# Kernel tuning notes

Measured on AMD Instinct MI355X. Metric: run time of the kernel, lower is better.

## Reference

```python
import jax, jax.numpy as jnp
import numpy as np

PS = 8  # window_size
LOCAL = 16  # split channels

def conv1x1(x, w, b):
    return jnp.einsum('oi,bihw->bohw', w, x) + b[None, :, None, None]

def dynamic_local(x, w1, b1, w2, b2, k):
    # x: (B, C, H, W); dynamic per-(batch,channel) depthwise conv with generated kernels
    B, C, H, W = x.shape
    pooled = x.mean((2, 3))                      # (B, C) adaptive avg pool to 1x1
    h = jax.nn.relu(pooled @ w1.T + b1)
    kern = (h @ w2.T + b2).reshape(B, C, k, k)   # per-sample depthwise kernels
    def per_batch(xb, kb):
        return jax.lax.conv_general_dilated(
            xb[None], kb[:, None], (1, 1), 'SAME',
            feature_group_count=C,
            dimension_numbers=('NCHW', 'OIHW', 'NCHW'))[0]
    return jax.vmap(per_batch)(x, kern)

def channel_layernorm(x, w, b, eps=1e-6):
    # LayerNorm over channel dim (torch module's non-channels_last path)
    u = x.mean(1, keepdims=True)
    s = ((x - u) ** 2).mean(1, keepdims=True)
    xn = (x - u) / jnp.sqrt(s + eps)
    return w[None, :, None, None] * xn + b[None, :, None, None]

def fsas(x, hid_w, hid_b, dw_w, dw_b, ln_w, ln_b, out_w, out_b):
    hidden = conv1x1(x, hid_w, hid_b)
    mid = hidden.shape[1]
    dw = jax.lax.conv_general_dilated(
        hidden, dw_w[:, None], (1, 1), 'SAME',
        feature_group_count=mid,
        dimension_numbers=('NCHW', 'OIHW', 'NCHW')) + dw_b[None, :, None, None]
    q, k, v = jnp.split(dw, 3, axis=1)
    B, C, H, W = q.shape
    def patch(t):
        # (B,C,H,W) -> (B,C,H/ps,W/ps,ps,ps)
        return t.reshape(B, C, H // PS, PS, W // PS, PS).transpose(0, 1, 2, 4, 3, 5)
    qf = jnp.fft.rfft2(patch(q))
    kf = jnp.fft.rfft2(patch(k))
    out = jnp.fft.irfft2(qf * kf, s=(PS, PS))
    out = out.transpose(0, 1, 2, 4, 3, 5).reshape(B, C, H, W)
    out = channel_layernorm(out, ln_w, ln_b)
    return conv1x1(v * out, out_w, out_b)


def setup_inputs() -> dict:
    key = jax.random.key(0)
    ks = jax.random.split(key, 12)
    s = 0.02
    return {
        'x': jax.random.normal(ks[0], (4, 64, 256, 256), jnp.float32),
        'dl1_w1': jax.random.normal(ks[1], (16, 16), jnp.float32) * s,
        'dl1_b1': jnp.zeros((16,), jnp.float32),
        'dl1_w2': jax.random.normal(ks[2], (144, 16), jnp.float32) * s,
        'dl1_b2': jnp.zeros((144,), jnp.float32),
        'dl2_w1': jax.random.normal(ks[3], (16, 16), jnp.float32) * s,
        'dl2_b1': jnp.zeros((16,), jnp.float32),
        'dl2_w2': jax.random.normal(ks[4], (400, 16), jnp.float32) * s,
        'dl2_b2': jnp.zeros((400,), jnp.float32),
        'fs_hid_w': jax.random.normal(ks[5], (144, 48), jnp.float32) * s,
        'fs_hid_b': jnp.zeros((144,), jnp.float32),
        'fs_dw_w': jax.random.normal(ks[6], (144, 3, 3), jnp.float32) * s,
        'fs_dw_b': jnp.zeros((144,), jnp.float32),
        'fs_ln_w': jnp.ones((48,), jnp.float32),
        'fs_ln_b': jnp.zeros((48,), jnp.float32),
        'fs_out_w': jax.random.normal(ks[7], (48, 48), jnp.float32) * s,
        'fs_out_b': jnp.zeros((48,), jnp.float32),
        'last_w': jax.random.normal(ks[8], (64, 64), jnp.float32) * s,
        'last_b': jnp.zeros((64,), jnp.float32),
    }


def reference(x, dl1_w1, dl1_b1, dl1_w2, dl1_b2, dl2_w1, dl2_b1, dl2_w2, dl2_b2,
              fs_hid_w, fs_hid_b, fs_dw_w, fs_dw_b, fs_ln_w, fs_ln_b,
              fs_out_w, fs_out_b, last_w, last_b):
    x1, x2 = x[:, :LOCAL], x[:, LOCAL:]
    x1 = dynamic_local(x1, dl1_w1, dl1_b1, dl1_w2, dl1_b2, 3)
    x1 = dynamic_local(x1, dl2_w1, dl2_b1, dl2_w2, dl2_b2, 5)
    x2 = fsas(x2, fs_hid_w, fs_hid_b, fs_dw_w, fs_dw_b, fs_ln_w, fs_ln_b, fs_out_w, fs_out_b)
    return conv1x1(jnp.concatenate([x1, x2], axis=1), last_w, last_b)
```

## Files before the change

### kernel.cpp

```cpp
#include <hip/hip_runtime.h>

typedef _Float16 h2 __attribute__((ext_vector_type(2)));
typedef _Float16 h4 __attribute__((ext_vector_type(4)));
typedef _Float16 h8 __attribute__((ext_vector_type(8)));
typedef float f4 __attribute__((ext_vector_type(4)));
typedef unsigned int u32;
typedef u32 u32x2 __attribute__((ext_vector_type(2)));
typedef u32 u32x4 __attribute__((ext_vector_type(4)));

__device__ __forceinline__ h2 bch2(u32 v) { return __builtin_bit_cast(h2, v); }

__device__ __forceinline__ float warpsum(float v) {
    for (int off = 32; off > 0; off >>= 1) v += __shfl_down(v, off);
    return v;
}

__device__ __forceinline__ int sswz(int p, int k) {
    return p * 64 + ((((k >> 3) ^ (p >> 3)) & 7) << 3) + (k & 7);
}

__global__ __launch_bounds__(256) void k_prep(const float* __restrict__ hid_w,
                                              const float* __restrict__ out_w,
                                              const float* __restrict__ last_w,
                                              _Float16* __restrict__ hwH,
                                              _Float16* __restrict__ owlwH) {
    int t = blockIdx.x * 256 + threadIdx.x;
    int stride = gridDim.x * 256;
    for (int i = t; i < 10368; i += stride) {
        int n = i / 72, k = i - n * 72;
        hwH[i] = (k < 48) ? (_Float16)hid_w[n * 48 + k] : (_Float16)0.f;
    }
    for (int i = t; i < 3456; i += stride) {
        int n = i / 72, k = i - n * 72;
        owlwH[i] = (k < 48) ? (_Float16)out_w[n * 48 + k] : (_Float16)0.f;
    }
    for (int i = t; i < 4608; i += stride) {
        int n = i / 72, k = i - n * 72;
        owlwH[3456 + i] = (k < 64) ? (_Float16)last_w[n * 64 + k] : (_Float16)0.f;
    }
}

__global__ __launch_bounds__(256) void k_pool(const float* __restrict__ x, float* __restrict__ pooled1) {
    int bid = blockIdx.x;
    int b = bid >> 4, c = bid & 15;
    const float* base = x + (size_t)(b * 64 + c) * 65536;
    float s = 0.f;
    for (int i = threadIdx.x; i < 16384; i += 256) {
        float4 v = ((const float4*)base)[i];
        s += v.x + v.y + v.z + v.w;
    }
    __shared__ float red[4];
    s = warpsum(s);
    if ((threadIdx.x & 63) == 0) red[threadIdx.x >> 6] = s;
    __syncthreads();
    if (threadIdx.x == 0) pooled1[bid] = (red[0] + red[1] + red[2] + red[3]) * (1.f / 65536.f);
}

__global__ __launch_bounds__(256) void k_kern1(const float* __restrict__ pooled1,
                                               const float* __restrict__ w1, const float* __restrict__ b1,
                                               const float* __restrict__ w2, const float* __restrict__ b2,
                                               float* __restrict__ kern1) {
    __shared__ float h[64];
    int t = threadIdx.x;
    if (t < 64) {
        int b = t >> 4, j = t & 15;
        float a = b1[j];
        for (int i = 0; i < 16; ++i) a += pooled1[b * 16 + i] * w1[j * 16 + i];
        h[t] = fmaxf(a, 0.f);
    }
    __syncthreads();
    for (int i = t; i < 576; i += 256) {
        int b = i / 144, o = i - b * 144;
        float a = b2[o];
        for (int j = 0; j < 16; ++j) a += h[b * 16 + j] * w2[o * 16 + j];
        kern1[i] = a;
    }
}

__global__ __launch_bounds__(256) void k_dw3(const float* __restrict__ x,
                                             const float* __restrict__ kern1,
                                             float* __restrict__ y1, float* __restrict__ rowsum) {
    __shared__ float tile[10][258];
    __shared__ float red[8][4];
    int bid = blockIdx.x;
    int rb = bid & 31, bc = bid >> 5;
    int b = bc >> 4, c = bc & 15;
    int row0 = rb << 3;
    int col = threadIdx.x;
    const float* xc = x + ((size_t)(b * 64 + c) << 16);
#pragma unroll
    for (int j = 0; j < 10; ++j) {
        int r = row0 - 1 + j;
        tile[j][col + 1] = ((unsigned)r < 256u) ? xc[(r << 8) + col] : 0.f;
    }
    if (col < 10) { tile[col][0] = 0.f; tile[col][257] = 0.f; }
    const float* k9 = kern1 + b * 144 + c * 9;
    float kk[9];
#pragma unroll
    for (int i = 0; i < 9; ++i) kk[i] = k9[i];
    __syncthreads();
#pragma unroll
    for (int j = 0; j < 8; ++j) {
        float acc = 0.f;
#pragma unroll
        for (int dy = 0; dy < 3; ++dy)
#pragma unroll
            for (int dx = 0; dx < 3; ++dx)
                acc += kk[dy * 3 + dx] * tile[j + dy][col + dx];
        y1[((size_t)bc << 16) + ((row0 + j) << 8) + col] = acc;
        float s = warpsum(acc);
        if ((col & 63) == 0) red[j][col >> 6] = s;
    }
    __syncthreads();
    if (col < 8) rowsum[bc * 256 + row0 + col] = red[col][0] + red[col][1] + red[col][2] + red[col][3];
}

__global__ __launch_bounds__(256) void k_kern2(const float* __restrict__ rowsum,
                                               const float* __restrict__ w1, const float* __restrict__ b1,
                                               const float* __restrict__ w2, const float* __restrict__ b2,
                                               float* __restrict__ kern2) {
    __shared__ float ps[256];
    __shared__ float p2[64];
    __shared__ float h[64];
    int t = threadIdx.x;
    {
        int pair = t >> 2, seg = t & 3;
        const float* rs = rowsum + pair * 256 + seg * 64;
        float s = 0.f;
        for (int j = 0; j < 64; ++j) s += rs[j];
        ps[t] = s;
    }
    __syncthreads();
    if (t < 64) p2[t] = (ps[t * 4] + ps[t * 4 + 1] + ps[t * 4 + 2] + ps[t * 4 + 3]) * (1.f / 65536.f);
    __syncthreads();
    if (t < 64) {
        int b = t >> 4, j = t & 15;
        float a = b1[j];
        for (int i = 0; i < 16; ++i) a += p2[b * 16 + i] * w1[j * 16 + i];
        h[t] = fmaxf(a, 0.f);
    }
    __syncthreads();
    for (int i = t; i < 1600; i += 256) {
        int b = i / 400, o = i - b * 400;
        float a = b2[o];
        for (int j = 0; j < 16; ++j) a += h[b * 16 + j] * w2[o * 16 + j];
        kern2[i] = a;
    }
}

__global__ __launch_bounds__(256) void k_dw5(const float* __restrict__ y1,
                                             const float* __restrict__ kern2,
                                             float* __restrict__ x1o) {
    __shared__ float tile[12][260];
    int bid = blockIdx.x;
    int rb = bid & 31, bc = bid >> 5;
    int b = bc >> 4, c = bc & 15;
    int row0 = rb << 3;
    int col = threadIdx.x;
    const float* yc = y1 + ((size_t)bc << 16);
#pragma unroll
    for (int j = 0; j < 12; ++j) {
        int r = row0 - 2 + j;
        tile[j][col + 2] = ((unsigned)r < 256u) ? yc[(r << 8) + col] : 0.f;
    }
    if (col < 12) { tile[col][0] = 0.f; tile[col][1] = 0.f; tile[col][258] = 0.f; tile[col][259] = 0.f; }
    const float* k25 = kern2 + b * 400 + c * 25;
    float kk[25];
#pragma unroll
    for (int i = 0; i < 25; ++i) kk[i] = k25[i];
    __syncthreads();
#pragma unroll
    for (int j = 0; j < 8; ++j) {
        float acc = 0.f;
#pragma unroll
        for (int dy = 0; dy < 5; ++dy)
#pragma unroll
            for (int dx = 0; dx < 5; ++dx)
                acc += kk[dy * 5 + dx] * tile[j + dy][col + dx];
        x1o[((size_t)bc << 16) + ((row0 + j) << 8) + col] = acc;
    }
}

__global__ __launch_bounds__(512, 6) void k_fsas(const float* __restrict__ x,
                                                 const _Float16* __restrict__ hwH, const float* __restrict__ hid_b,
                                                 const float* __restrict__ dw_w, const float* __restrict__ dw_b,
                                                 const float* __restrict__ ln_w, const float* __restrict__ ln_b,
                                                 const _Float16* __restrict__ owlwH, const float* __restrict__ out_b,
                                                 const float* __restrict__ last_b,
                                                 const float* __restrict__ x1o, float* __restrict__ out) {
    __shared__ __align__(16) _Float16 Sbig[17856];
    __shared__ __align__(16) _Float16 qk[6144];
    __shared__ __align__(16) float pstat[128];

    _Float16* Abuf  = Sbig;
    _Float16* hbuf  = Sbig;
    _Float16* fbuf  = Sbig;
    float*    lnp   = (float*)(Sbig + 4608);
    _Float16* outb  = Sbig + 6656;
    _Float16* qbuf  = qk;
    _Float16* kbuf  = qk + 3072;
    _Float16* sbufA = qk;

    int tid = threadIdx.x;
    int lane = tid & 63;
    int wave = __builtin_amdgcn_readfirstlane(tid >> 6);
    int bid = blockIdx.x;
    int swz = ((bid & 7) << 9) | (bid >> 3);
    int b = swz >> 10;
    int rem = swz & 1023;
    int row0 = (rem >> 5) << 3, col0 = (rem & 31) << 3;

    int l16 = lane & 15, lhi = lane >> 4;
    int mb = wave * 16 + (lhi << 2);
    bool vok[4];
#pragma unroll
    for (int r = 0; r < 4; ++r) {
        int m = mb + r;
        int yv = m / 12, xv = m - yv * 12;
        vok[r] = (m < 120) && (xv < 10) &&
                 ((unsigned)(row0 - 1 + yv) < 256u) && ((unsigned)(col0 - 1 + xv) < 256u);
    }

    if (tid < 480) {
        int k2 = tid / 20, r20 = tid - (tid / 20) * 20;
        int y = r20 >> 1, xh = r20 & 1;
        int gy = row0 - 1 + y;
        bool rowok = (unsigned)gy < 256u;
        const float* xa = x + ((size_t)(b * 64 + 16 + 2 * k2) << 16) + ((size_t)(gy & 255) << 8);
        const float* xb = xa + 65536;
#pragma unroll
        for (int xx = 0; xx < 6; ++xx) {
            int xv = xh * 6 + xx;
            int gx = col0 - 1 + xv;
            bool ok = rowok && (xv < 10) && ((unsigned)gx < 256u);
            float va = ok ? xa[gx] : 0.f;
            float vb = ok ? xb[gx] : 0.f;
            *(h2*)(Abuf + (y * 12 + xv) * 72 + 2 * k2) = (h2){(_Float16)va, (_Float16)vb};
        }
    }
    if (tid < 240) {
        int p = tid >> 1, kb = 48 + ((tid & 1) << 3);
        *(h8*)(Abuf + p * 72 + kb) = (h8)(_Float16)0.f;
    }
    __syncthreads();

    int arow = wave * 16 + l16;
    h8 a0 = *(const h8*)(Abuf + arow * 72 + (lhi << 3));
    h8 a1 = *(const h8*)(Abuf + arow * 72 + 32 + (lhi << 3));
    __syncthreads();

    float xr[8];
    int fpx = lane, fgrp = wave - 6;
    if (wave >= 6) {
        size_t gp = ((size_t)(row0 + (fpx >> 3)) << 8) + col0 + (fpx & 7);
#pragma unroll
        for (int j = 0; j < 8; ++j)
            xr[j] = x1o[((size_t)(b * 16 + fgrp * 8 + j) << 16) + gp];
    }

#pragma unroll
    for (int nt = 0; nt < 9; ++nt) {
        const _Float16* wr = hwH + (nt * 16 + l16) * 72 + (lhi << 3);
        h8 b0 = *(const h8*)(wr);
        h8 b1 = *(const h8*)(wr + 32);
        float bias = hid_b[nt * 16 + l16];
        f4 acc = {bias, bias, bias, bias};
        acc = __builtin_amdgcn_mfma_f32_16x16x32_f16(a0, b0, acc, 0, 0, 0);
        acc = __builtin_amdgcn_mfma_f32_16x16x32_f16(a1, b1, acc, 0, 0, 0);
        int n_l = nt * 16 + l16;
        if (mb < 120) {
            h2 p0 = {vok[0] ? (_Float16)acc[0] : (_Float16)0.f, vok[1] ? (_Float16)acc[1] : (_Float16)0.f};
            h2 p1 = {vok[2] ? (_Float16)acc[2] : (_Float16)0.f, vok[3] ? (_Float16)acc[3] : (_Float16)0.f};
            *(h2*)(hbuf + n_l * 124 + mb) = p0;
            *(h2*)(hbuf + n_l * 124 + mb + 2) = p1;
        }
    }
    __syncthreads();

    int dch = tid >> 3, drow = tid & 7;
    h8 vreg;
    auto dw_row = [&](int ch, int row, float o[8]) {
        const float* dwp = dw_w + ch * 9;
        float bias = dw_b[ch];
#pragma unroll
        for (int xx = 0; xx < 8; ++xx) o[xx] = bias;
        const _Float16* hb = hbuf + ch * 124 + row * 12;
#pragma unroll
        for (int dy = 0; dy < 3; ++dy) {
            u32x2 A2 = *(const u32x2*)(hb + dy * 12);
            u32x2 B2 = *(const u32x2*)(hb + dy * 12 + 4);
            u32 r89 = *(const u32*)(hb + dy * 12 + 8);
            u32 r01 = A2.x, r23 = A2.y, r45 = B2.x, r67 = B2.y;
            u32 s12 = __builtin_amdgcn_alignbit(r23, r01, 16);
            u32 s34 = __builtin_amdgcn_alignbit(r45, r23, 16);
            u32 s56 = __builtin_amdgcn_alignbit(r67, r45, 16);
            u32 s78 = __builtin_amdgcn_alignbit(r89, r67, 16);
            _Float16 w0 = (_Float16)dwp[dy * 3], w1 = (_Float16)dwp[dy * 3 + 1], w2 = (_Float16)dwp[dy * 3 + 2];
            h2 w01 = {w0, w1};
            h2 w2lo = {w2, (_Float16)0.f};
            h2 w2hi = {(_Float16)0.f, w2};
            o[0] = __builtin_amdgcn_fdot2(w01, bch2(r01), o[0], false);
            o[0] = __builtin_amdgcn_fdot2(w2lo, bch2(r23), o[0], false);
            o[1] = __builtin_amdgcn_fdot2(w01, bch2(s12), o[1], false);
            o[1] = __builtin_amdgcn_fdot2(w2lo, bch2(s34), o[1], false);
            o[2] = __builtin_amdgcn_fdot2(w01, bch2(r23), o[2], false);
            o[2] = __builtin_amdgcn_fdot2(w2lo, bch2(r45), o[2], false);
            o[3] = __builtin_amdgcn_fdot2(w01, bch2(s34), o[3], false);
            o[3] = __builtin_amdgcn_fdot2(w2lo, bch2(s56), o[3], false);
            o[4] = __builtin_amdgcn_fdot2(w01, bch2(r45), o[4], false);
            o[4] = __builtin_amdgcn_fdot2(w2lo, bch2(r67), o[4], false);
            o[5] = __builtin_amdgcn_fdot2(w01, bch2(s56), o[5], false);
            o[5] = __builtin_amdgcn_fdot2(w2lo, bch2(s78), o[5], false);
            o[6] = __builtin_amdgcn_fdot2(w01, bch2(r67), o[6], false);
            o[6] = __builtin_amdgcn_fdot2(w2lo, bch2(r89), o[6], false);
            o[7] = __builtin_amdgcn_fdot2(w01, bch2(s78), o[7], false);
            o[7] = __builtin_amdgcn_fdot2(w2hi, bch2(r89), o[7], false);
        }
    };
    if (tid < 384) {
        float oq[8];
        dw_row(dch, drow, oq);
        h8 qv;
#pragma unroll
        for (int xx = 0; xx < 8; ++xx) qv[xx] = (_Float16)oq[xx];
        *(h8*)(qbuf + dch * 64 + drow * 8) = qv;
        float ov[8];
        dw_row(96 + dch, drow, ov);
#pragma unroll
        for (int xx = 0; xx < 8; ++xx) vreg[xx] = (_Float16)ov[xx];
    } else {
        int j0 = (tid - 384) * 3;
#pragma unroll
        for (int i = 0; i < 3; ++i) {
            int j = j0 + i;
            int kc = j >> 3, kr = j & 7;
            float ok8[8];
            dw_row(48 + kc, kr, ok8);
            h8 krv;
#pragma unroll
            for (int t2 = 0; t2 < 8; ++t2) krv[t2] = (_Float16)ok8[(8 - t2) & 7];
            *(h8*)(kbuf + kc * 64 + kr * 8) = krv;
        }
    }
    __syncthreads();

    float co[8];
    if (tid < 384) {
        int ch = dch, m = drow;
#pragma unroll
        for (int n = 0; n < 8; ++n) co[n] = 0.f;
#pragma unroll
        for (int i8 = 0; i8 < 8; ++i8) {
            int r = (m - i8) & 7;
            u32x4 qv = *(const u32x4*)(qbuf + ch * 64 + i8 * 8);
            u32x4 ev = *(const u32x4*)(kbuf + ch * 64 + r * 8);
            h2 qp[4] = {bch2(qv.x), bch2(qv.y), bch2(qv.z), bch2(qv.w)};
            h2 ep[4] = {bch2(ev.x), bch2(ev.y), bch2(ev.z), bch2(ev.w)};
            h2 op[4] = {bch2(__builtin_amdgcn_alignbit(ev.x, ev.w, 16)),
                        bch2(__builtin_amdgcn_alignbit(ev.y, ev.x, 16)),
                        bch2(__builtin_amdgcn_alignbit(ev.z, ev.y, 16)),
                        bch2(__builtin_amdgcn_alignbit(ev.w, ev.z, 16))};
#pragma unroll
            for (int u = 0; u < 4; ++u)
#pragma unroll
                for (int a = 0; a < 4; ++a) {
                    co[2 * u]     = __builtin_amdgcn_fdot2(qp[a], ep[(a - u) & 3], co[2 * u], false);
                    co[2 * u + 1] = __builtin_amdgcn_fdot2(qp[a], op[(a - u) & 3], co[2 * u + 1], false);
                }
        }
#pragma unroll
        for (int v = 0; v < 4; ++v)
            *(h2*)(outb + dch * 66 + drow * 8 + 2 * v) = (h2){(_Float16)co[2 * v], (_Float16)co[2 * v + 1]};
    } else {
        h8 fv;
#pragma unroll
        for (int j = 0; j < 8; ++j) fv[j] = (_Float16)xr[j];
        *(h8*)(fbuf + fpx * 72 + fgrp * 8) = fv;
    }
    __syncthreads();

    {
        int px = tid & 63, g = tid >> 6;
        float s = 0.f, ss = 0.f;
#pragma unroll
        for (int cc = 0; cc < 6; ++cc) {
            float v = (float)outb[(g * 6 + cc) * 66 + px];
            s += v; ss += v * v;
        }
        lnp[g * 64 + px] = s;
        lnp[512 + g * 64 + px] = ss;
    }
    __syncthreads();
    if (tid < 64) {
        float s = 0.f, ss = 0.f;
#pragma unroll
        for (int g = 0; g < 8; ++g) { s += lnp[g * 64 + tid]; ss += lnp[512 + g * 64 + tid]; }
        float mu = s * (1.f / 48.f);
        float var = ss * (1.f / 48.f) - mu * mu;
        pstat[tid * 2] = mu;
        pstat[tid * 2 + 1] = rsqrtf(var + 1e-6f);
    }
    __syncthreads();

    if (tid < 384) {
        float lw = ln_w[dch], lb = ln_b[dch];
        const float* ps = pstat + drow * 16;
#pragma unroll
        for (int n = 0; n < 8; ++n) {
            float mu = ps[2 * n], inv = ps[2 * n + 1];
            float lnv = lw * ((co[n] - mu) * inv) + lb;
            sbufA[sswz(drow * 8 + n, dch)] = (_Float16)((float)vreg[n] * lnv);
        }
    }
    *(h2*)(sbufA + sswz(lane, 48 + (wave << 1))) = (h2){(_Float16)0.f, (_Float16)0.f};
    __syncthreads();

    for (int t = wave; t < 12; t += 8) {
        int mt = t / 3, nt = t - mt * 3;
        int row5 = mt * 16 + l16;
        h8 c0 = *(const h8*)(sbufA + sswz(row5, lhi << 3));
        h8 c1 = *(const h8*)(sbufA + sswz(row5, 32 + (lhi << 3)));
        h8 d0 = *(const h8*)(owlwH + nt * 1152 + l16 * 72 + (lhi << 3));
        h8 d1 = *(const h8*)(owlwH + nt * 1152 + l16 * 72 + 32 + (lhi << 3));
        float bias = out_b[nt * 16 + l16];
        f4 acc = {bias, bias, bias, bias};
        acc = __builtin_amdgcn_mfma_f32_16x16x32_f16(c0, d0, acc, 0, 0, 0);
        acc = __builtin_amdgcn_mfma_f32_16x16x32_f16(c1, d1, acc, 0, 0, 0);
        int n5 = nt * 16 + l16;
        int pb = mt * 16 + (lhi << 2);
#pragma unroll
        for (int r = 0; r < 4; ++r)
            fbuf[(pb + r) * 72 + 16 + n5] = (_Float16)acc[r];
    }
    __syncthreads();

    for (int t = wave; t < 16; t += 8) {
        int mt = t >> 2, nt = t & 3;
        int row6 = mt * 16 + l16;
        h8 c0 = *(const h8*)(fbuf + row6 * 72 + (lhi << 3));
        h8 c1 = *(const h8*)(fbuf + row6 * 72 + 32 + (lhi << 3));
        h8 d0 = *(const h8*)(owlwH + 3456 + nt * 1152 + l16 * 72 + (lhi << 3));
        h8 d1 = *(const h8*)(owlwH + 3456 + nt * 1152 + l16 * 72 + 32 + (lhi << 3));
        float bias = last_b[nt * 16 + l16];
        f4 acc = {bias, bias, bias, bias};
        acc = __builtin_amdgcn_mfma_f32_16x16x32_f16(c0, d0, acc, 0, 0, 0);
        acc = __builtin_amdgcn_mfma_f32_16x16x32_f16(c1, d1, acc, 0, 0, 0);
        int ch = nt * 16 + l16;
        int px0 = mt * 16 + (lhi << 2);
        float4 val = {acc[0], acc[1], acc[2], acc[3]};
        *(float4*)(out + ((size_t)(b * 64 + ch) << 16) + ((size_t)(row0 + (px0 >> 3)) << 8) + col0 + (px0 & 7)) = val;
    }
}

extern "C" void kernel_launch(void* const* d_in, const int* in_sizes, int n_in,
                              void* d_out, int out_size, void* d_ws, size_t ws_size,
                              hipStream_t stream) {
    const float* x      = (const float*)d_in[0];
    const float* dl1_w1 = (const float*)d_in[1];
    const float* dl1_b1 = (const float*)d_in[2];
    const float* dl1_w2 = (const float*)d_in[3];
    const float* dl1_b2 = (const float*)d_in[4];
    const float* dl2_w1 = (const float*)d_in[5];
    const float* dl2_b1 = (const float*)d_in[6];
    const float* dl2_w2 = (const float*)d_in[7];
    const float* dl2_b2 = (const float*)d_in[8];
    const float* hid_w  = (const float*)d_in[9];
    const float* hid_b  = (const float*)d_in[10];
    const float* dw_w   = (const float*)d_in[11];
    const float* dw_b   = (const float*)d_in[12];
    const float* ln_w   = (const float*)d_in[13];
    const float* ln_b   = (const float*)d_in[14];
    const float* out_w  = (const float*)d_in[15];
    const float* out_b  = (const float*)d_in[16];
    const float* last_w = (const float*)d_in[17];
    const float* last_b = (const float*)d_in[18];
    float* out = (float*)d_out;

    float* ws      = (float*)d_ws;
    float* pooled1 = ws;
    float* kern1   = ws + 64;
    float* rowsum  = ws + 1024;
    float* kern2   = ws + 17408;
    _Float16* hwH   = (_Float16*)(ws + 19008);
    _Float16* owlwH = (_Float16*)(ws + 24192);
    float* y1      = ws + 32768;
    float* x1o     = ws + 32768 + 4194304;

    k_prep <<<8,    256, 0, stream>>>(hid_w, out_w, last_w, hwH, owlwH);
    k_pool <<<64,   256, 0, stream>>>(x, pooled1);
    k_kern1<<<1,    256, 0, stream>>>(pooled1, dl1_w1, dl1_b1, dl1_w2, dl1_b2, kern1);
    k_dw3  <<<2048, 256, 0, stream>>>(x, kern1, y1, rowsum);
    k_kern2<<<1,    256, 0, stream>>>(rowsum, dl2_w1, dl2_b1, dl2_w2, dl2_b2, kern2);
    k_dw5  <<<2048, 256, 0, stream>>>(y1, kern2, x1o);
    k_fsas <<<4096, 512, 0, stream>>>(x, hwH, hid_b, dw_w, dw_b, ln_w, ln_b,
                                      owlwH, out_b, last_b, x1o, out);
}
```

Measured before the change: 167.2 us.

## Fold fsas output projection into final 1x1 conv and compute layernorm stats via shuffles

Precomputes last_w[:,16:] @ out_w and a combined bias in the prep kernel, which removes the separate out-projection MFMA stage and one barrier from the fused kernel. Per-pixel layernorm sums are now reduced with wave-level xor shuffles inside the circular-convolution waves rather than through a staging buffer, two LDS passes and extra syncs. The folded weights are rounded to fp16 after the product, so numerics shift slightly, and the shuffle reduction adds register pressure in the convolution waves.

```diff
diff --git a/kernel.cpp b/kernel.cpp
--- a/kernel.cpp
+++ b/kernel.cpp
@@ -22,21 +22,31 @@
 __global__ __launch_bounds__(256) void k_prep(const float* __restrict__ hid_w,
                                               const float* __restrict__ out_w,
                                               const float* __restrict__ last_w,
+                                              const float* __restrict__ out_b,
+                                              const float* __restrict__ last_b,
                                               _Float16* __restrict__ hwH,
-                                              _Float16* __restrict__ owlwH) {
+                                              _Float16* __restrict__ lwC,
+                                              float* __restrict__ bias_comb) {
     int t = blockIdx.x * 256 + threadIdx.x;
     int stride = gridDim.x * 256;
     for (int i = t; i < 10368; i += stride) {
         int n = i / 72, k = i - n * 72;
         hwH[i] = (k < 48) ? (_Float16)hid_w[n * 48 + k] : (_Float16)0.f;
     }
-    for (int i = t; i < 3456; i += stride) {
-        int n = i / 72, k = i - n * 72;
-        owlwH[i] = (k < 48) ? (_Float16)out_w[n * 48 + k] : (_Float16)0.f;
-    }
-    for (int i = t; i < 4608; i += stride) {
-        int n = i / 72, k = i - n * 72;
-        owlwH[3456 + i] = (k < 64) ? (_Float16)last_w[n * 64 + k] : (_Float16)0.f;
+    for (int i = t; i < 4096; i += stride) {
+        int n = i >> 6, k = i & 63;
+        float v;
+        if (k < 16) v = last_w[n * 64 + k];
+        else {
+            v = 0.f;
+            for (int o = 0; o < 48; ++o) v += last_w[n * 64 + 16 + o] * out_w[o * 48 + (k - 16)];
+        }
+        lwC[i] = (_Float16)v;
+    }
+    for (int n = t; n < 64; n += stride) {
+        float v = last_b[n];
+        for (int o = 0; o < 48; ++o) v += last_w[n * 64 + 16 + o] * out_b[o];
+        bias_comb[n] = v;
     }
 }
 
@@ -185,21 +195,17 @@
                                                  const _Float16* __restrict__ hwH, const float* __restrict__ hid_b,
                                                  const float* __restrict__ dw_w, const float* __restrict__ dw_b,
                                                  const float* __restrict__ ln_w, const float* __restrict__ ln_b,
-                                                 const _Float16* __restrict__ owlwH, const float* __restrict__ out_b,
-                                                 const float* __restrict__ last_b,
+                                                 const _Float16* __restrict__ lwC, const float* __restrict__ bias_comb,
                                                  const float* __restrict__ x1o, float* __restrict__ out) {
     __shared__ __align__(16) _Float16 Sbig[17856];
     __shared__ __align__(16) _Float16 qk[6144];
-    __shared__ __align__(16) float pstat[128];
-
-    _Float16* Abuf  = Sbig;
-    _Float16* hbuf  = Sbig;
-    _Float16* fbuf  = Sbig;
-    float*    lnp   = (float*)(Sbig + 4608);
-    _Float16* outb  = Sbig + 6656;
-    _Float16* qbuf  = qk;
-    _Float16* kbuf  = qk + 3072;
-    _Float16* sbufA = qk;
+
+    _Float16* Abuf = Sbig;
+    _Float16* hbuf = Sbig;
+    _Float16* fbuf = Sbig;
+    float*    lnp2 = (float*)(Sbig + 4608);
+    _Float16* qbuf = qk;
+    _Float16* kbuf = qk + 3072;
 
     int tid = threadIdx.x;
     int lane = tid & 63;
@@ -250,9 +256,9 @@
     __syncthreads();
 
     float xr[8];
-    int fpx = lane, fgrp = wave - 6;
+    int fgrp = wave - 6;
     if (wave >= 6) {
-        size_t gp = ((size_t)(row0 + (fpx >> 3)) << 8) + col0 + (fpx & 7);
+        size_t gp = ((size_t)(row0 + (lane >> 3)) << 8) + col0 + (lane & 7);
 #pragma unroll
         for (int j = 0; j < 8; ++j)
             xr[j] = x1o[((size_t)(b * 16 + fgrp * 8 + j) << 16) + gp];
@@ -368,80 +374,66 @@
                     co[2 * u + 1] = __builtin_amdgcn_fdot2(qp[a], op[(a - u) & 3], co[2 * u + 1], false);
                 }
         }
-#pragma unroll
-        for (int v = 0; v < 4; ++v)
-            *(h2*)(outb + dch * 66 + drow * 8 + 2 * v) = (h2){(_Float16)co[2 * v], (_Float16)co[2 * v + 1]};
+        float s[8], ss[8];
+#pragma unroll
+        for (int n = 0; n < 8; ++n) { s[n] = co[n]; ss[n] = co[n] * co[n]; }
+#pragma unroll
+        for (int off = 8; off < 64; off <<= 1) {
+#pragma unroll
+            for (int n = 0; n < 8; ++n) {
+                s[n] += __shfl_xor(s[n], off);
+                ss[n] += __shfl_xor(ss[n], off);
+            }
+        }
+        int c8 = lane >> 3, mm = lane & 7;
+        int p = mm * 8 + c8;
+        float2 pv = {0.f, 0.f};
+#pragma unroll
+        for (int n = 0; n < 8; ++n) if (n == c8) { pv.x = s[n]; pv.y = ss[n]; }
+        *(float2*)(lnp2 + wave * 128 + p * 2) = pv;
     } else {
         h8 fv;
 #pragma unroll
         for (int j = 0; j < 8; ++j) fv[j] = (_Float16)xr[j];
-        *(h8*)(fbuf + fpx * 72 + fgrp * 8) = fv;
-    }
-    __syncthreads();
-
-    {
-        int px = tid & 63, g = tid >> 6;
-        float s = 0.f, ss = 0.f;
-#pragma unroll
-        for (int cc = 0; cc < 6; ++cc) {
-            float v = (float)outb[(g * 6 + cc) * 66 + px];
-            s += v; ss += v * v;
-        }
-        lnp[g * 64 + px] = s;
-        lnp[512 + g * 64 + px] = ss;
-    }
-    __syncthreads();
-    if (tid < 64) {
-        float s = 0.f, ss = 0.f;
-#pragma unroll
-        for (int g = 0; g < 8; ++g) { s += lnp[g * 64 + tid]; ss += lnp[512 + g * 64 + tid]; }
-        float mu = s * (1.f / 48.f);
-        float var = ss * (1.f / 48.f) - mu * mu;
-        pstat[tid * 2] = mu;
-        pstat[tid * 2 + 1] = rsqrtf(var + 1e-6f);
+        *(h8*)(fbuf + sswz(lane, fgrp * 8)) = fv;
     }
     __syncthreads();
 
     if (tid < 384) {
+        int m = drow;
+        float sAcc[8], ssAcc[8];
+#pragma unroll
+        for (int n = 0; n < 8; ++n) { sAcc[n] = 0.f; ssAcc[n] = 0.f; }
+#pragma unroll
+        for (int w = 0; w < 6; ++w) {
+            const float* lp = lnp2 + w * 128 + m * 16;
+#pragma unroll
+            for (int j = 0; j < 4; ++j) {
+                f4 v4 = *(const f4*)(lp + j * 4);
+                sAcc[2 * j] += v4[0];  ssAcc[2 * j] += v4[1];
+                sAcc[2 * j + 1] += v4[2]; ssAcc[2 * j + 1] += v4[3];
+            }
+        }
         float lw = ln_w[dch], lb = ln_b[dch];
-        const float* ps = pstat + drow * 16;
 #pragma unroll
         for (int n = 0; n < 8; ++n) {
-            float mu = ps[2 * n], inv = ps[2 * n + 1];
+            float mu = sAcc[n] * (1.f / 48.f);
+            float var = ssAcc[n] * (1.f / 48.f) - mu * mu;
+            float inv = rsqrtf(var + 1e-6f);
             float lnv = lw * ((co[n] - mu) * inv) + lb;
-            sbufA[sswz(drow * 8 + n, dch)] = (_Float16)((float)vreg[n] * lnv);
-        }
-    }
-    *(h2*)(sbufA + sswz(lane, 48 + (wave << 1))) = (h2){(_Float16)0.f, (_Float16)0.f};
-    __syncthreads();
-
-    for (int t = wave; t < 12; t += 8) {
-        int mt = t / 3, nt = t - mt * 3;
-        int row5 = mt * 16 + l16;
-        h8 c0 = *(const h8*)(sbufA + sswz(row5, lhi << 3));
-        h8 c1 = *(const h8*)(sbufA + sswz(row5, 32 + (lhi << 3)));
-        h8 d0 = *(const h8*)(owlwH + nt * 1152 + l16 * 72 + (lhi << 3));
-        h8 d1 = *(const h8*)(owlwH + nt * 1152 + l16 * 72 + 32 + (lhi << 3));
-        float bias = out_b[nt * 16 + l16];
-        f4 acc = {bias, bias, bias, bias};
-        acc = __builtin_amdgcn_mfma_f32_16x16x32_f16(c0, d0, acc, 0, 0, 0);
-        acc = __builtin_amdgcn_mfma_f32_16x16x32_f16(c1, d1, acc, 0, 0, 0);
-        int n5 = nt * 16 + l16;
-        int pb = mt * 16 + (lhi << 2);
-#pragma unroll
-        for (int r = 0; r < 4; ++r)
-            fbuf[(pb + r) * 72 + 16 + n5] = (_Float16)acc[r];
+            fbuf[sswz(m * 8 + n, 16 + dch)] = (_Float16)((float)vreg[n] * lnv);
+        }
     }
     __syncthreads();
 
     for (int t = wave; t < 16; t += 8) {
         int mt = t >> 2, nt = t & 3;
         int row6 = mt * 16 + l16;
-        h8 c0 = *(const h8*)(fbuf + row6 * 72 + (lhi << 3));
-        h8 c1 = *(const h8*)(fbuf + row6 * 72 + 32 + (lhi << 3));
-        h8 d0 = *(const h8*)(owlwH + 3456 + nt * 1152 + l16 * 72 + (lhi << 3));
-        h8 d1 = *(const h8*)(owlwH + 3456 + nt * 1152 + l16 * 72 + 32 + (lhi << 3));
-        float bias = last_b[nt * 16 + l16];
+        h8 c0 = *(const h8*)(fbuf + sswz(row6, lhi << 3));
+        h8 c1 = *(const h8*)(fbuf + sswz(row6, 32 + (lhi << 3)));
+        h8 d0 = *(const h8*)(lwC + (nt * 16 + l16) * 64 + (lhi << 3));
+        h8 d1 = *(const h8*)(lwC + (nt * 16 + l16) * 64 + 32 + (lhi << 3));
+        float bias = bias_comb[nt * 16 + l16];
         f4 acc = {bias, bias, bias, bias};
         acc = __builtin_amdgcn_mfma_f32_16x16x32_f16(c0, d0, acc, 0, 0, 0);
         acc = __builtin_amdgcn_mfma_f32_16x16x32_f16(c1, d1, acc, 0, 0, 0);
@@ -482,16 +474,17 @@
     float* rowsum  = ws + 1024;
     float* kern2   = ws + 17408;
     _Float16* hwH   = (_Float16*)(ws + 19008);
-    _Float16* owlwH = (_Float16*)(ws + 24192);
+    _Float16* lwC   = (_Float16*)(ws + 24192);
+    float* bias_comb = ws + 26240;
     float* y1      = ws + 32768;
     float* x1o     = ws + 32768 + 4194304;
 
-    k_prep <<<8,    256, 0, stream>>>(hid_w, out_w, last_w, hwH, owlwH);
+    k_prep <<<8,    256, 0, stream>>>(hid_w, out_w, last_w, out_b, last_b, hwH, lwC, bias_comb);
     k_pool <<<64,   256, 0, stream>>>(x, pooled1);
     k_kern1<<<1,    256, 0, stream>>>(pooled1, dl1_w1, dl1_b1, dl1_w2, dl1_b2, kern1);
     k_dw3  <<<2048, 256, 0, stream>>>(x, kern1, y1, rowsum);
     k_kern2<<<1,    256, 0, stream>>>(rowsum, dl2_w1, dl2_b1, dl2_w2, dl2_b2, kern2);
     k_dw5  <<<2048, 256, 0, stream>>>(y1, kern2, x1o);
     k_fsas <<<4096, 512, 0, stream>>>(x, hwH, hid_b, dw_w, dw_b, ln_w, ln_b,
-                                      owlwH, out_b, last_b, x1o, out);
-}
+                                      lwC, bias_comb, x1o, out);
+}
```

New measurement: 184.2 us. +10.2%, slower.
